# Optimization experiments

Hardware: AMD Instinct MI355X
Metric: run time of the kernel (lower is better)

The kernel has to match this reference:

```python
import jax, jax.numpy as jnp
import numpy as np

B, N, C, H = 8, 512, 64, 128
T, K = 10, 2                       # dilation threshold and skip divisor
TAUS = (0.25, 0.5, 0.75)
WTS = (0.25, 0.5, 0.25)
EPS_GIN = 0.0                      # (1 + eps) * x, eps buffer
AVG_DEG = 32.0


def setup_inputs() -> dict:
    key = jax.random.key(0)
    ks = jax.random.split(key, 6)
    x = jax.random.normal(ks[0], (B, N, C), jnp.float32)
    u = jax.random.uniform(ks[1], (B, N, N))
    a = u < (AVG_DEG / N)
    adj = jnp.maximum(a, jnp.swapaxes(a, 1, 2)).astype(jnp.float32)  # symmetric binary adjacency
    mask = jax.random.bernoulli(ks[2], 0.9, (B, N))
    W1 = jax.random.normal(ks[3], (C, H), jnp.float32) / np.float32(np.sqrt(C))
    b1 = jnp.zeros((H,), jnp.float32)
    W2 = jax.random.normal(ks[4], (H, C), jnp.float32) / np.float32(np.sqrt(H))
    b2 = jnp.zeros((C,), jnp.float32)
    return {"x": x, "adj": adj, "mask": mask, "W1": W1, "b1": b1, "W2": W2, "b2": b2}


def reference(x, adj, mask, W1, b1, W2, b2):
    Bc, Nc, Cc = x.shape
    eye = jnp.eye(Nc, dtype=bool)
    adj_ = jnp.where(eye, 1.0, adj)                 # add_loop=True: force self loops
    # ---- vectorized dilation (replaces the per-(b,n) python loop) ----
    neigh = (adj_ > 0) & (~eye)                     # neighbors excluding self [B,N,N]
    ni = neigh.astype(jnp.int32)
    rank = jnp.cumsum(ni, axis=-1) - ni             # exclusive rank of m among n's sorted neighbors
    nb = ni.sum(-1)                                 # [B,N] neighbor count (w/o self)
    skip = jnp.where(nb > T, (nb + K - 1) // K, 1)  # ceil(nb/k) if nb > T else 1 (linear mode, layer 1)
    skip = jnp.maximum(skip, 1)
    sk = skip[:, :, None]
    # remove relative indices skip-1, 2*skip-1, ... when skip > 1, only for masked-in nodes
    rem = neigh & (sk > 1) & ((rank % sk) == (sk - 1)) & mask[:, :, None]
    rem = rem | jnp.swapaxes(rem, 1, 2)             # symmetric removal
    adj_d = jnp.where(rem, 0.0, adj_)
    # ---- masked quantile aggregation over neighbors (== nanquantile) ----
    nd = adj_d > 0                                  # includes self loop -> at least 1 valid
    vals = jnp.where(nd[..., None], x[:, None, :, :], jnp.inf)  # [B,N,M,C]; invalid -> +inf
    s = jnp.sort(vals, axis=2)                      # valid values first, ascending
    nv = nd.sum(2)                                  # [B,N] valid count per node
    agg = jnp.zeros_like(x)
    for tau, w in zip(TAUS, WTS):                   # small fixed loop over quantiles
        pos = jnp.asarray(tau, x.dtype) * jnp.maximum(nv - 1, 0).astype(x.dtype)
        lo = jnp.floor(pos).astype(jnp.int32)
        hi = jnp.ceil(pos).astype(jnp.int32)
        frac = (pos - lo.astype(x.dtype))[..., None]
        idx_lo = jnp.broadcast_to(lo[:, :, None, None], (Bc, Nc, 1, Cc))
        idx_hi = jnp.broadcast_to(hi[:, :, None, None], (Bc, Nc, 1, Cc))
        v_lo = jnp.take_along_axis(s, idx_lo, axis=2)[:, :, 0, :]
        v_hi = jnp.take_along_axis(s, idx_hi, axis=2)[:, :, 0, :]
        agg = agg + jnp.asarray(w, x.dtype) * (v_lo + frac * (v_hi - v_lo))
    agg = jnp.where(nv[..., None] > 0, agg, 0.0)    # nan_to_num for empty rows
    out = (1.0 + EPS_GIN) * x + agg
    h = jax.nn.relu(out @ W1 + b1)                  # GIN MLP: Linear-ReLU-Linear
    y = h @ W2 + b2
    return y * mask[..., None].astype(y.dtype)
```

## Files before the change

kernel.cpp:

```cpp
#include <hip/hip_runtime.h>
#include <cstdint>

#define B_ 8
#define N_ 512
#define C_ 64
#define H_ 128
#define T_ 10
#define K_ 2
#define WPR 16
#define NVMAX 96
#define TT 8

__device__ inline uint32_t fkey(float v) {
    uint32_t bits = __float_as_uint(v);
    return (bits & 0x80000000u) ? ~bits : (bits | 0x80000000u);
}
__device__ inline float fdec(uint32_t key) {
    uint32_t ok = (key & 0xFFFFFF00u) | 0x80u;
    uint32_t bits = (ok & 0x80000000u) ? (ok ^ 0x80000000u) : ~ok;
    return __uint_as_float(bits);
}

__device__ __forceinline__ uint32_t bittr32(uint32_t x, int kk) {
    const int ss[5] = {16, 8, 4, 2, 1};
    const uint32_t mm[5] = {0x0000FFFFu, 0x00FF00FFu, 0x0F0F0F0Fu,
                            0x33333333u, 0x55555555u};
#pragma unroll
    for (int t = 0; t < 5; ++t) {
        int s = ss[t]; uint32_t Ms = mm[t];
        uint32_t y = (uint32_t)__shfl_xor((int)x, s, 64);
        x = (kk & s) ? ((x & ~Ms) | ((y & ~Ms) >> s))
                     : ((x & Ms)  | ((y & Ms)  << s));
    }
    return x;
}

__global__ __launch_bounds__(256) void pass1_keep(const float* __restrict__ adj,
                                                  const int* __restrict__ mask,
                                                  uint32_t* __restrict__ keepbits) {
    int wid = threadIdx.x >> 6, lane = threadIdx.x & 63;
    int row = blockIdx.x * 4 + wid;
    int i = row & (N_ - 1);
    const float4* arow4 = (const float4*)(adj + (size_t)row * N_);
    float4 a0 = arow4[lane * 2];
    float4 a1 = arow4[lane * 2 + 1];
    float av[8] = {a0.x, a0.y, a0.z, a0.w, a1.x, a1.y, a1.z, a1.w};

    int flags = 0, cnt = 0;
    int jbase = lane * 8;
#pragma unroll
    for (int k = 0; k < 8; ++k) {
        int j = jbase + k;
        bool ng = (j != i) && (av[k] > 0.0f);
        flags |= ((int)ng) << k;
        cnt += (int)ng;
    }
    int inc = cnt;
#pragma unroll
    for (int d = 1; d < 64; d <<= 1) {
        int o = __shfl_up(inc, d, 64);
        if (lane >= d) inc += o;
    }
    int excl = inc - cnt;
    int nb = __shfl(inc, 63, 64);
    int skip = (nb > T_) ? ((nb + K_ - 1) / K_) : 1;
    if (skip < 1) skip = 1;
    int maski = mask[row];

    unsigned remb = 0;
    if (skip > 1 && maski != 0) {
        int r = excl;
#pragma unroll
        for (int k = 0; k < 8; ++k) {
            if ((flags >> k) & 1) {
                if (r % skip == skip - 1) remb |= 1u << k;
                ++r;
            }
        }
    }
    unsigned diagb = (i >= jbase && i < jbase + 8) ? (1u << (i - jbase)) : 0u;
    unsigned keepb = (((unsigned)flags | diagb) & ~remb) & 0xFFu;

    unsigned p0 = __shfl((int)keepb, (lane & 15) * 4 + 0, 64);
    unsigned p1 = __shfl((int)keepb, (lane & 15) * 4 + 1, 64);
    unsigned p2 = __shfl((int)keepb, (lane & 15) * 4 + 2, 64);
    unsigned p3 = __shfl((int)keepb, (lane & 15) * 4 + 3, 64);
    if (lane < WPR) {
        uint32_t w = (p0 & 0xFFu) | ((p1 & 0xFFu) << 8) |
                     ((p2 & 0xFFu) << 16) | ((p3 & 0xFFu) << 24);
        keepbits[(size_t)row * WPR + lane] = w;
    }
}

__global__ __launch_bounds__(256) void pass1p5_transpose_and(uint32_t* __restrict__ kb) {
    int bb = blockIdx.x;
    int tid = threadIdx.x;
    int g32 = tid >> 5;
    int kk  = tid & 31;
    __shared__ uint32_t w1p[N_ * 17];
    uint32_t* g = kb + (size_t)bb * N_ * WPR;

    for (int idx = tid; idx < N_ * WPR; idx += 256)
        w1p[(idx >> 4) * 17 + (idx & 15)] = g[idx];
    __syncthreads();

    for (int unit = g32; unit < 136; unit += 8) {
        int R = 0, u = unit;
        while (u >= 16 - R) { u -= 16 - R; ++R; }
        int G = R + u;
        uint32_t A  = w1p[(32 * R + kk) * 17 + G];
        uint32_t Bt = (R == G) ? A : w1p[(32 * G + kk) * 17 + R];
        uint32_t At  = bittr32(A, kk);
        uint32_t Btt = bittr32(Bt, kk);
        w1p[(32 * R + kk) * 17 + G] = A & Btt;
        if (R != G) w1p[(32 * G + kk) * 17 + R] = Bt & At;
    }
    __syncthreads();

    for (int idx = tid; idx < N_ * WPR; idx += 256)
        g[idx] = w1p[(idx >> 4) * 17 + (idx & 15)];
}

__global__ __launch_bounds__(256) void pass2_quant_mlp(
        const float* __restrict__ x,
        const int* __restrict__ mask, const uint32_t* __restrict__ keepbits,
        const float* __restrict__ W1, const float* __restrict__ b1,
        const float* __restrict__ W2, const float* __restrict__ b2,
        float* __restrict__ out) {
    int row = blockIdx.x;
    int b = row >> 9, i = row & (N_ - 1);
    int tid = threadIdx.x;
    int lane = tid & 63;
    int q = tid >> 6;

    __shared__ unsigned short kept[NVMAX];
    __shared__ int s_cnt;
    __shared__ uint32_t keys[NVMAX * C_];
    __shared__ float selv[6][C_];
    float* mlp_buf = (float*)keys;

    if (tid == 0) s_cnt = 0;
    __syncthreads();

    const float* xb = x + (size_t)b * N_ * C_;
    float xself = xb[(size_t)i * C_ + lane];
    int mv = mask[row];

    const uint32_t* krow = keepbits + (size_t)row * WPR;
    for (int jb = 0; jb < N_; jb += 256) {
        int j = jb + tid;
        bool keep = (krow[j >> 5] >> (j & 31)) & 1u;
        unsigned long long bal = __ballot(keep);
        int base = 0;
        if (lane == 0 && bal) base = atomicAdd(&s_cnt, __popcll(bal));
        base = __shfl(base, 0, 64);
        if (keep) {
            int pos = __popcll(bal & ((1ull << lane) - 1ull));
            int p = base + pos;
            if (p < NVMAX) kept[p] = (unsigned short)j;
        }
    }
    __syncthreads();
    int nv = s_cnt;
    if (nv > NVMAX) nv = NVMAX;

    for (int t = q; t < nv; t += 4) {
        float v = xb[(size_t)kept[t] * C_ + lane];
        keys[t * C_ + lane] = (fkey(v) & 0xFFFFFF00u) | (uint32_t)t;
    }

    float nm1 = (float)((nv - 1 > 0) ? nv - 1 : 0);
    float p0 = 0.25f * nm1, p1 = 0.5f * nm1, p2 = 0.75f * nm1;
    int rr0 = (int)floorf(p0), rr1 = (int)ceilf(p0);
    int rr2 = (int)floorf(p1), rr3 = (int)ceilf(p1);
    int rr4 = (int)floorf(p2), rr5 = (int)ceilf(p2);
    __syncthreads();

    const uint32_t* kcol = keys + lane;

    for (int base = 0; base < nv; base += 32) {
        int tbase = base + q * TT;
        if (tbase >= nv) continue;
        uint32_t k[TT];
        int rs_a[TT], rs_b[TT];
#pragma unroll
        for (int m = 0; m < TT; ++m) {
            int t = tbase + m;
            k[m] = (t < nv) ? kcol[t * C_] : 0xFFFFFFFFu;
            rs_a[m] = 0; rs_b[m] = 0;
        }
        int u = 0;
#pragma unroll 2
        for (; u + 1 < nv; u += 2) {
            uint32_t w0 = kcol[u * C_];
            uint32_t w1v = kcol[(u + 1) * C_];
#pragma unroll
            for (int m = 0; m < TT; ++m) {
                rs_a[m] += (int)(w0 < k[m]);
                rs_b[m] += (int)(w1v < k[m]);
            }
        }
        if (u < nv) {
            uint32_t w0 = kcol[u * C_];
#pragma unroll
            for (int m = 0; m < TT; ++m) rs_a[m] += (int)(w0 < k[m]);
        }
#pragma unroll
        for (int m = 0; m < TT; ++m) {
            int rs = rs_a[m] + rs_b[m];
            bool h0 = rs == rr0, h1 = rs == rr1, h2 = rs == rr2;
            bool h3 = rs == rr3, h4 = rs == rr4, h5 = rs == rr5;
            if (h0 | h1 | h2 | h3 | h4 | h5) {
                float fv = fdec(k[m]);
                if (h0) selv[0][lane] = fv;
                if (h1) selv[1][lane] = fv;
                if (h2) selv[2][lane] = fv;
                if (h3) selv[3][lane] = fv;
                if (h4) selv[4][lane] = fv;
                if (h5) selv[5][lane] = fv;
            }
        }
    }
    __syncthreads();

    if (tid < C_) {
        float f0 = p0 - floorf(p0), f1 = p1 - floorf(p1), f2 = p2 - floorf(p2);
        float agg = 0.25f * (selv[0][tid] + f0 * (selv[1][tid] - selv[0][tid]));
        agg      += 0.5f  * (selv[2][tid] + f1 * (selv[3][tid] - selv[2][tid]));
        agg      += 0.25f * (selv[4][tid] + f2 * (selv[5][tid] - selv[4][tid]));
        mlp_buf[tid] = xself + agg;
    }
    __syncthreads();

    {
        int hcol = tid & 127, chalf = tid >> 7;
        float acc = 0.0f;
#pragma unroll 4
        for (int c = 0; c < 32; ++c) {
            int c0 = chalf * 32 + c;
            acc += mlp_buf[c0] * W1[c0 * H_ + hcol];
        }
        mlp_buf[192 + tid] = acc;
    }
    __syncthreads();
    if (tid < H_) {
        float h = mlp_buf[192 + tid] + mlp_buf[192 + tid + 128] + b1[tid];
        mlp_buf[64 + tid] = h > 0.0f ? h : 0.0f;
    }
    __syncthreads();

    {
        int ycol = tid & 63, kq = tid >> 6;
        float acc = 0.0f;
#pragma unroll 4
        for (int kk = 0; kk < 32; ++kk) {
            int k0 = kq * 32 + kk;
            acc += mlp_buf[64 + k0] * W2[k0 * C_ + ycol];
        }
        mlp_buf[192 + tid] = acc;
    }
    __syncthreads();
    if (tid < C_) {
        float maskf = (mv != 0) ? 1.0f : 0.0f;
        float y = b2[tid] + mlp_buf[192 + tid] + mlp_buf[192 + tid + 64]
                + mlp_buf[192 + tid + 128] + mlp_buf[192 + tid + 192];
        out[(size_t)row * C_ + tid] = y * maskf;
    }
}

extern "C" void kernel_launch(void* const* d_in, const int* in_sizes, int n_in,
                              void* d_out, int out_size, void* d_ws, size_t ws_size,
                              hipStream_t stream) {
    const float* x   = (const float*)d_in[0];
    const float* adj = (const float*)d_in[1];
    const int*  mask = (const int*)d_in[2];
    const float* W1  = (const float*)d_in[3];
    const float* b1  = (const float*)d_in[4];
    const float* W2  = (const float*)d_in[5];
    const float* b2  = (const float*)d_in[6];
    float* out = (float*)d_out;

    uint32_t* keepbits = (uint32_t*)d_ws;

    hipLaunchKernelGGL(pass1_keep, dim3(B_ * N_ / 4), dim3(256), 0, stream,
                       adj, mask, keepbits);
    hipLaunchKernelGGL(pass1p5_transpose_and, dim3(B_), dim3(256), 0, stream,
                       keepbits);
    hipLaunchKernelGGL(pass2_quant_mlp, dim3(B_ * N_), dim3(256), 0, stream,
                       x, mask, keepbits, W1, b1, W2, b2, out);
}
```

Baseline: 177.1 us.

## Replace bit-transpose kernel with atomic scatter of removals and widen pass2 blocks

Drops the separate transpose-and-AND kernel, which ran only 8 blocks. Instead, pass1 scatters each removed edge's transposed bit into a zeroed remT bitmap with atomicOr, and pass2 combines keepbits & ~remT when it builds each row's neighbor list. Pass2 also moves from 256 to 512 threads per block, so each block takes 64 key candidates per rank step and splits the MLP reductions into more partial sums. The cost is an extra memset, global atomics, and a heavier per-block register and scheduling footprint.

```diff
diff --git a/kernel.cpp b/kernel.cpp
--- a/kernel.cpp
+++ b/kernel.cpp
@@ -21,25 +21,13 @@
     return __uint_as_float(bits);
 }
 
-__device__ __forceinline__ uint32_t bittr32(uint32_t x, int kk) {
-    const int ss[5] = {16, 8, 4, 2, 1};
-    const uint32_t mm[5] = {0x0000FFFFu, 0x00FF00FFu, 0x0F0F0F0Fu,
-                            0x33333333u, 0x55555555u};
-#pragma unroll
-    for (int t = 0; t < 5; ++t) {
-        int s = ss[t]; uint32_t Ms = mm[t];
-        uint32_t y = (uint32_t)__shfl_xor((int)x, s, 64);
-        x = (kk & s) ? ((x & ~Ms) | ((y & ~Ms) >> s))
-                     : ((x & Ms)  | ((y & Ms)  << s));
-    }
-    return x;
-}
-
 __global__ __launch_bounds__(256) void pass1_keep(const float* __restrict__ adj,
                                                   const int* __restrict__ mask,
-                                                  uint32_t* __restrict__ keepbits) {
+                                                  uint32_t* __restrict__ keepbits,
+                                                  uint32_t* __restrict__ remT) {
     int wid = threadIdx.x >> 6, lane = threadIdx.x & 63;
     int row = blockIdx.x * 4 + wid;
+    int bb = row >> 9;
     int i = row & (N_ - 1);
     const float4* arow4 = (const float4*)(adj + (size_t)row * N_);
     float4 a0 = arow4[lane * 2];
@@ -80,6 +68,13 @@
     }
     unsigned diagb = (i >= jbase && i < jbase + 8) ? (1u << (i - jbase)) : 0u;
     unsigned keepb = (((unsigned)flags | diagb) & ~remb) & 0xFFu;
+
+    unsigned rb = remb;
+    while (rb) {
+        int k = __ffs(rb) - 1; rb &= rb - 1;
+        int j = jbase + k;
+        atomicOr(&remT[(size_t)(bb * N_ + j) * WPR + (i >> 5)], 1u << (i & 31));
+    }
 
     unsigned p0 = __shfl((int)keepb, (lane & 15) * 4 + 0, 64);
     unsigned p1 = __shfl((int)keepb, (lane & 15) * 4 + 1, 64);
@@ -92,38 +87,10 @@
     }
 }
 
-__global__ __launch_bounds__(256) void pass1p5_transpose_and(uint32_t* __restrict__ kb) {
-    int bb = blockIdx.x;
-    int tid = threadIdx.x;
-    int g32 = tid >> 5;
-    int kk  = tid & 31;
-    __shared__ uint32_t w1p[N_ * 17];
-    uint32_t* g = kb + (size_t)bb * N_ * WPR;
-
-    for (int idx = tid; idx < N_ * WPR; idx += 256)
-        w1p[(idx >> 4) * 17 + (idx & 15)] = g[idx];
-    __syncthreads();
-
-    for (int unit = g32; unit < 136; unit += 8) {
-        int R = 0, u = unit;
-        while (u >= 16 - R) { u -= 16 - R; ++R; }
-        int G = R + u;
-        uint32_t A  = w1p[(32 * R + kk) * 17 + G];
-        uint32_t Bt = (R == G) ? A : w1p[(32 * G + kk) * 17 + R];
-        uint32_t At  = bittr32(A, kk);
-        uint32_t Btt = bittr32(Bt, kk);
-        w1p[(32 * R + kk) * 17 + G] = A & Btt;
-        if (R != G) w1p[(32 * G + kk) * 17 + R] = Bt & At;
-    }
-    __syncthreads();
-
-    for (int idx = tid; idx < N_ * WPR; idx += 256)
-        g[idx] = w1p[(idx >> 4) * 17 + (idx & 15)];
-}
-
-__global__ __launch_bounds__(256) void pass2_quant_mlp(
+__global__ __launch_bounds__(512) void pass2_quant_mlp(
         const float* __restrict__ x,
         const int* __restrict__ mask, const uint32_t* __restrict__ keepbits,
+        const uint32_t* __restrict__ remT,
         const float* __restrict__ W1, const float* __restrict__ b1,
         const float* __restrict__ W2, const float* __restrict__ b2,
         float* __restrict__ out) {
@@ -146,10 +113,11 @@
     float xself = xb[(size_t)i * C_ + lane];
     int mv = mask[row];
 
-    const uint32_t* krow = keepbits + (size_t)row * WPR;
-    for (int jb = 0; jb < N_; jb += 256) {
-        int j = jb + tid;
-        bool keep = (krow[j >> 5] >> (j & 31)) & 1u;
+    {
+        int j = tid;
+        uint32_t w = keepbits[(size_t)row * WPR + (j >> 5)]
+                   & ~remT[(size_t)row * WPR + (j >> 5)];
+        bool keep = (w >> (j & 31)) & 1u;
         unsigned long long bal = __ballot(keep);
         int base = 0;
         if (lane == 0 && bal) base = atomicAdd(&s_cnt, __popcll(bal));
@@ -164,7 +132,7 @@
     int nv = s_cnt;
     if (nv > NVMAX) nv = NVMAX;
 
-    for (int t = q; t < nv; t += 4) {
+    for (int t = q; t < nv; t += 8) {
         float v = xb[(size_t)kept[t] * C_ + lane];
         keys[t * C_ + lane] = (fkey(v) & 0xFFFFFF00u) | (uint32_t)t;
     }
@@ -178,7 +146,7 @@
 
     const uint32_t* kcol = keys + lane;
 
-    for (int base = 0; base < nv; base += 32) {
+    for (int base = 0; base < nv; base += 64) {
         int tbase = base + q * TT;
         if (tbase >= nv) continue;
         uint32_t k[TT];
@@ -233,18 +201,19 @@
     __syncthreads();
 
     {
-        int hcol = tid & 127, chalf = tid >> 7;
+        int hcol = tid & 127, cq = tid >> 7;
         float acc = 0.0f;
 #pragma unroll 4
-        for (int c = 0; c < 32; ++c) {
-            int c0 = chalf * 32 + c;
+        for (int c = 0; c < 16; ++c) {
+            int c0 = cq * 16 + c;
             acc += mlp_buf[c0] * W1[c0 * H_ + hcol];
         }
         mlp_buf[192 + tid] = acc;
     }
     __syncthreads();
     if (tid < H_) {
-        float h = mlp_buf[192 + tid] + mlp_buf[192 + tid + 128] + b1[tid];
+        float h = b1[tid] + mlp_buf[192 + tid] + mlp_buf[320 + tid]
+                + mlp_buf[448 + tid] + mlp_buf[576 + tid];
         mlp_buf[64 + tid] = h > 0.0f ? h : 0.0f;
     }
     __syncthreads();
@@ -253,8 +222,8 @@
         int ycol = tid & 63, kq = tid >> 6;
         float acc = 0.0f;
 #pragma unroll 4
-        for (int kk = 0; kk < 32; ++kk) {
-            int k0 = kq * 32 + kk;
+        for (int kk = 0; kk < 16; ++kk) {
+            int k0 = kq * 16 + kk;
             acc += mlp_buf[64 + k0] * W2[k0 * C_ + ycol];
         }
         mlp_buf[192 + tid] = acc;
@@ -262,8 +231,9 @@
     __syncthreads();
     if (tid < C_) {
         float maskf = (mv != 0) ? 1.0f : 0.0f;
-        float y = b2[tid] + mlp_buf[192 + tid] + mlp_buf[192 + tid + 64]
-                + mlp_buf[192 + tid + 128] + mlp_buf[192 + tid + 192];
+        float y = b2[tid];
+#pragma unroll
+        for (int e = 0; e < 8; ++e) y += mlp_buf[192 + tid + 64 * e];
         out[(size_t)row * C_ + tid] = y * maskf;
     }
 }
@@ -281,11 +251,11 @@
     float* out = (float*)d_out;
 
     uint32_t* keepbits = (uint32_t*)d_ws;
-
+    uint32_t* remT     = keepbits + (size_t)B_ * N_ * WPR;
+
+    hipMemsetAsync(remT, 0, (size_t)B_ * N_ * WPR * sizeof(uint32_t), stream);
     hipLaunchKernelGGL(pass1_keep, dim3(B_ * N_ / 4), dim3(256), 0, stream,
-                       adj, mask, keepbits);
-    hipLaunchKernelGGL(pass1p5_transpose_and, dim3(B_), dim3(256), 0, stream,
-                       keepbits);
-    hipLaunchKernelGGL(pass2_quant_mlp, dim3(B_ * N_), dim3(256), 0, stream,
-                       x, mask, keepbits, W1, b1, W2, b2, out);
-}
+                       adj, mask, keepbits, remT);
+    hipLaunchKernelGGL(pass2_quant_mlp, dim3(B_ * N_), dim3(512), 0, stream,
+                       x, mask, keepbits, remT, W1, b1, W2, b2, out);
+}
```

Result: faster. 162.2 us (-8.4%).
